# Kernel optimization log

Hardware: AMD Instinct MI355X
Metric: run time of the kernel (lower is better)

## Reference

```python
import jax, jax.numpy as jnp
import numpy as np

N = 50000      # nodes
E = 600000     # edges (avg degree 12)
D = 128        # in_dim == hidden_dim
C = 47         # n_classes
L = 3          # n_layers


def setup_inputs() -> dict:
    key = jax.random.key(0)
    ks = jax.random.split(key, 8)
    s = 1.0 / np.sqrt(D)
    return {
        "features": jax.random.normal(ks[0], (N, D), jnp.float32),
        "src": jax.random.randint(ks[1], (E,), 0, N, jnp.int32),
        "dst": jax.random.randint(ks[2], (E,), 0, N, jnp.int32),
        "w_self": jax.random.normal(ks[3], (L, D, D), jnp.float32) * s,
        "w_neigh": jax.random.normal(ks[4], (L, D, D), jnp.float32) * s,
        "b": jax.random.normal(ks[5], (L, D), jnp.float32) * s,
        "wc": jax.random.normal(ks[6], (D, C), jnp.float32) * s,
        "bc": jax.random.normal(ks[7], (C,), jnp.float32) * s,
    }


def reference(features, src, dst, w_self, w_neigh, b, wc, bc):
    # in-degree for mean aggregation (clamped to avoid div-by-zero)
    deg = jax.ops.segment_sum(jnp.ones((E,), features.dtype), dst, num_segments=N)
    inv_deg = 1.0 / jnp.maximum(deg, 1.0)  # [N]
    h = features
    for l in range(L):
        # SAGEConv (mean aggregator): gather src feats, mean-reduce onto dst
        msgs = jnp.take(h, src, axis=0)                       # [E, D]
        h_neigh = jax.ops.segment_sum(msgs, dst, num_segments=N) * inv_deg[:, None]  # [N, D]
        h = jax.nn.relu(h @ w_self[l] + h_neigh @ w_neigh[l] + b[l])
    logits = h @ wc + bc                                      # [N, C]
    return jax.nn.softmax(logits, axis=-1)
```

## Files before the change

### kernel.cpp

```cpp
#include <hip/hip_runtime.h>
#include <hip/hip_bf16.h>
#include <float.h>

#define DIM  128
#define NCLS 47
#define MAXD 64

typedef __attribute__((ext_vector_type(8))) short bf16x8;
typedef __attribute__((ext_vector_type(4))) float f32x4;

__device__ inline unsigned short bf16_rne(float v) {
  unsigned u = __float_as_uint(v);
  return (unsigned short)((u + 0x7FFFu + ((u >> 16) & 1u)) >> 16);
}

__device__ inline void split_bf16(float v, unsigned short& hi, unsigned short& lo) {
  unsigned int u = __float_as_uint(v);
  unsigned int r = (u + 0x7FFFu + ((u >> 16) & 1u)) >> 16;
  hi = (unsigned short)r;
  float hf = __uint_as_float(r << 16);
  float l = v - hf;
  unsigned int ul = __float_as_uint(l);
  unsigned int rl = (ul + 0x7FFFu + ((ul >> 16) & 1u)) >> 16;
  lo = (unsigned short)rl;
}

__device__ inline uint4 pack8(const unsigned short* h) {
  uint4 u;
  u.x = (unsigned)h[0] | ((unsigned)h[1] << 16);
  u.y = (unsigned)h[2] | ((unsigned)h[3] << 16);
  u.z = (unsigned)h[4] | ((unsigned)h[5] << 16);
  u.w = (unsigned)h[6] | ((unsigned)h[7] << 16);
  return u;
}

__global__ __launch_bounds__(256) void k_prep(const float* __restrict__ w_self,
                                              const float* __restrict__ w_neigh,
                                              const float* __restrict__ wc,
                                              const float* __restrict__ feat,
                                              uint4* __restrict__ Bhi,
                                              uint4* __restrict__ Blo,
                                              uint4* __restrict__ Chi,
                                              uint4* __restrict__ Clo,
                                              unsigned short* __restrict__ P0,
                                              unsigned short* __restrict__ P1,
                                              unsigned short* __restrict__ P2,
                                              int* __restrict__ cnt,
                                              int* __restrict__ eidx,
                                              int n, long total8) {
  int bid = blockIdx.x, tid = threadIdx.x;
  if (bid < 48) {
    int unit = bid * 4 + (tid >> 6);
    int lane = tid & 63;
    int lt = unit >> 6, rem = unit & 63, kt = rem >> 3, ct = rem & 7;
    int col = ct * 16 + (lane & 15);
    unsigned short h[8], lw[8];
#pragma unroll
    for (int j = 0; j < 8; ++j) {
      int kg = kt * 32 + (lane >> 4) * 8 + j;
      float v = (kg < 128) ? w_self[(size_t)lt * DIM * DIM + (size_t)kg * DIM + col]
                           : w_neigh[(size_t)lt * DIM * DIM + (size_t)(kg - 128) * DIM + col];
      split_bf16(v, h[j], lw[j]);
    }
    size_t idx = (((size_t)lt * 64 + kt * 8 + ct) * 64 + lane);
    Bhi[idx] = pack8(h);
    Blo[idx] = pack8(lw);
  } else if (bid < 51) {
    int unit = (bid - 48) * 4 + (tid >> 6);
    if (unit < 12) {
      int lane = tid & 63;
      int kt = unit / 3, ct = unit % 3;
      int col = ct * 16 + (lane & 15);
      unsigned short h[8], lw[8];
#pragma unroll
      for (int j = 0; j < 8; ++j) {
        int k = kt * 32 + (lane >> 4) * 8 + j;
        float v = (col < NCLS) ? wc[(size_t)k * NCLS + col] : 0.f;
        split_bf16(v, h[j], lw[j]);
      }
      size_t idx = (size_t)(kt * 3 + ct) * 64 + lane;
      Chi[idx] = pack8(h);
      Clo[idx] = pack8(lw);
    }
  } else {
    long i = (long)(bid - 51) * 256 + tid;
    if (i < n) cnt[i] = 0;
    if (i < total8) {
      const float* s = feat + i * 8;
      unsigned short h[8];
#pragma unroll
      for (int j = 0; j < 8; ++j) h[j] = bf16_rne(s[j]);
      *(uint4*)&P0[i * 8] = pack8(h);
      int4 sv = {n, n, n, n};
      ((int4*)eidx)[i] = sv;
    }
    if (bid == 51 && tid < 16) {
      uint4 z = {0u, 0u, 0u, 0u};
      ((uint4*)(P0 + (size_t)n * DIM))[tid] = z;
      ((uint4*)(P1 + (size_t)n * DIM))[tid] = z;
      ((uint4*)(P2 + (size_t)n * DIM))[tid] = z;
    }
  }
}

__global__ __launch_bounds__(256) void k_scatter4(const int* __restrict__ src,
                                                  const int* __restrict__ dst,
                                                  int* __restrict__ cnt,
                                                  int* __restrict__ eidx, int E) {
  int t = blockIdx.x * blockDim.x + threadIdx.x;
  int e0 = t * 4;
  if (e0 + 3 < E) {
    int4 d4 = *(const int4*)(dst + e0);
    int4 s4 = *(const int4*)(src + e0);
    int p0 = atomicAdd(&cnt[d4.x], 1);
    int p1 = atomicAdd(&cnt[d4.y], 1);
    int p2 = atomicAdd(&cnt[d4.z], 1);
    int p3 = atomicAdd(&cnt[d4.w], 1);
    if (p0 < MAXD) eidx[(size_t)d4.x * MAXD + p0] = s4.x;
    if (p1 < MAXD) eidx[(size_t)d4.y * MAXD + p1] = s4.y;
    if (p2 < MAXD) eidx[(size_t)d4.z * MAXD + p2] = s4.z;
    if (p3 < MAXD) eidx[(size_t)d4.w * MAXD + p3] = s4.w;
  } else {
    for (int e = e0; e < E; ++e) {
      int d = dst[e];
      int pos = atomicAdd(&cnt[d], 1);
      if (pos < MAXD) eidx[(size_t)d * MAXD + pos] = src[e];
    }
  }
}

__global__ __launch_bounds__(256) void k_agg9(const unsigned short* __restrict__ plane,
                                              unsigned short* __restrict__ hn,
                                              const int* __restrict__ cnt,
                                              const int* __restrict__ eidx, int n) {
  int node = blockIdx.x * 4 + (threadIdx.x >> 6);
  if (node >= n) return;
  int lane = threadIdx.x & 63;
  int g = lane >> 4, li = lane & 15;
  int d = cnt[node];
  int dcl = d < MAXD ? d : MAXD;
  int s = node * MAXD;
  int nch = (dcl + 15) >> 4;
  float acc[8];
#pragma unroll
  for (int k = 0; k < 8; ++k) acc[k] = 0.f;

  for (int c = 0; c < nch; ++c) {
    int base = s + c * 16 + g;
    int u0 = eidx[base];
    int u1 = eidx[base + 4];
    int u2 = eidx[base + 8];
    int u3 = eidx[base + 12];
    uint4 v0 = *(const uint4*)(plane + (size_t)u0 * DIM + li * 8);
    uint4 v1 = *(const uint4*)(plane + (size_t)u1 * DIM + li * 8);
    uint4 v2 = *(const uint4*)(plane + (size_t)u2 * DIM + li * 8);
    uint4 v3 = *(const uint4*)(plane + (size_t)u3 * DIM + li * 8);
    acc[0] += __uint_as_float(v0.x << 16); acc[1] += __uint_as_float(v0.x & 0xffff0000u);
    acc[2] += __uint_as_float(v0.y << 16); acc[3] += __uint_as_float(v0.y & 0xffff0000u);
    acc[4] += __uint_as_float(v0.z << 16); acc[5] += __uint_as_float(v0.z & 0xffff0000u);
    acc[6] += __uint_as_float(v0.w << 16); acc[7] += __uint_as_float(v0.w & 0xffff0000u);
    acc[0] += __uint_as_float(v1.x << 16); acc[1] += __uint_as_float(v1.x & 0xffff0000u);
    acc[2] += __uint_as_float(v1.y << 16); acc[3] += __uint_as_float(v1.y & 0xffff0000u);
    acc[4] += __uint_as_float(v1.z << 16); acc[5] += __uint_as_float(v1.z & 0xffff0000u);
    acc[6] += __uint_as_float(v1.w << 16); acc[7] += __uint_as_float(v1.w & 0xffff0000u);
    acc[0] += __uint_as_float(v2.x << 16); acc[1] += __uint_as_float(v2.x & 0xffff0000u);
    acc[2] += __uint_as_float(v2.y << 16); acc[3] += __uint_as_float(v2.y & 0xffff0000u);
    acc[4] += __uint_as_float(v2.z << 16); acc[5] += __uint_as_float(v2.z & 0xffff0000u);
    acc[6] += __uint_as_float(v2.w << 16); acc[7] += __uint_as_float(v2.w & 0xffff0000u);
    acc[0] += __uint_as_float(v3.x << 16); acc[1] += __uint_as_float(v3.x & 0xffff0000u);
    acc[2] += __uint_as_float(v3.y << 16); acc[3] += __uint_as_float(v3.y & 0xffff0000u);
    acc[4] += __uint_as_float(v3.z << 16); acc[5] += __uint_as_float(v3.z & 0xffff0000u);
    acc[6] += __uint_as_float(v3.w << 16); acc[7] += __uint_as_float(v3.w & 0xffff0000u);
  }
#pragma unroll
  for (int k = 0; k < 8; ++k) {
    acc[k] += __shfl_xor(acc[k], 16);
    acc[k] += __shfl_xor(acc[k], 32);
  }
  if (g == 0) {
    float idg = 1.0f / (float)(d > 1 ? d : 1);
    unsigned short hb[8];
#pragma unroll
    for (int k = 0; k < 8; ++k) hb[k] = bf16_rne(acc[k] * idg);
    *(uint4*)(hn + (size_t)node * DIM + li * 8) = pack8(hb);
  }
}

template <int LAST>
__global__ __launch_bounds__(256) void k_mm2(const unsigned short* __restrict__ plane,
                                             const unsigned short* __restrict__ hn,
                                             const uint4* __restrict__ Bhi,
                                             const uint4* __restrict__ Blo,
                                             const float* __restrict__ bias,
                                             unsigned short* __restrict__ oplane,
                                             const uint4* __restrict__ Chi,
                                             const uint4* __restrict__ Clo,
                                             const float* __restrict__ bc,
                                             float* __restrict__ out,
                                             int n) {
  __shared__ char U[34816];
  uint4* Bs = (uint4*)U;
  int tid = threadIdx.x, lane = tid & 63, w = tid >> 6;
  int rb = blockIdx.x * 128 + w * 32;

  f32x4 acc[2][8];
#pragma unroll
  for (int rf = 0; rf < 2; ++rf)
#pragma unroll
    for (int ct = 0; ct < 8; ++ct) acc[rf][ct] = (f32x4){0.f, 0.f, 0.f, 0.f};

  int r0 = rb + (lane & 15);      if (r0 > n - 1) r0 = n - 1;
  int r1 = rb + 16 + (lane & 15); if (r1 > n - 1) r1 = n - 1;
  int koff = (lane >> 4) * 8;
  const unsigned short* a0s = plane + (size_t)r0 * DIM + koff;
  const unsigned short* a1s = plane + (size_t)r1 * DIM + koff;
  const unsigned short* a0n = hn + (size_t)r0 * DIM + koff;
  const unsigned short* a1n = hn + (size_t)r1 * DIM + koff;

#define STAGE_B(kt_, buf_)                                                    \
  {                                                                           \
    const uint4* hsrc = Bhi + (size_t)(kt_) * 512;                            \
    const uint4* lsrc = Blo + (size_t)(kt_) * 512;                            \
    uint4* dstb = Bs + (size_t)(buf_) * 1024;                                 \
    dstb[tid]        = hsrc[tid];                                             \
    dstb[tid + 256]  = hsrc[tid + 256];                                       \
    dstb[tid + 512]  = lsrc[tid];                                             \
    dstb[tid + 768]  = lsrc[tid + 256];                                       \
  }

  STAGE_B(0, 0);
  __syncthreads();

#pragma unroll
  for (int kt = 0; kt < 8; ++kt) {
    if (kt < 7) STAGE_B(kt + 1, (kt + 1) & 1);
    int buf = kt & 1;
    bf16x8 a0 = (kt < 4) ? *(const bf16x8*)(a0s + kt * 32)
                         : *(const bf16x8*)(a0n + (kt - 4) * 32);
    bf16x8 a1 = (kt < 4) ? *(const bf16x8*)(a1s + kt * 32)
                         : *(const bf16x8*)(a1n + (kt - 4) * 32);
    const uint4* bb = Bs + (size_t)buf * 1024;
#pragma unroll
    for (int ct = 0; ct < 8; ++ct) {
      bf16x8 bh = *(const bf16x8*)&bb[ct * 64 + lane];
      bf16x8 bl = *(const bf16x8*)&bb[512 + ct * 64 + lane];
      acc[0][ct] = __builtin_amdgcn_mfma_f32_16x16x32_bf16(a0, bh, acc[0][ct], 0, 0, 0);
      acc[0][ct] = __builtin_amdgcn_mfma_f32_16x16x32_bf16(a0, bl, acc[0][ct], 0, 0, 0);
      acc[1][ct] = __builtin_amdgcn_mfma_f32_16x16x32_bf16(a1, bh, acc[1][ct], 0, 0, 0);
      acc[1][ct] = __builtin_amdgcn_mfma_f32_16x16x32_bf16(a1, bl, acc[1][ct], 0, 0, 0);
    }
    __syncthreads();
  }
#undef STAGE_B

  char* tw = U + (size_t)w * 32 * 272;
#pragma unroll
  for (int rf = 0; rf < 2; ++rf)
#pragma unroll
    for (int ct = 0; ct < 8; ++ct) {
      float bv = bias[ct * 16 + (lane & 15)];
#pragma unroll
      for (int q = 0; q < 4; ++q) {
        float val = fmaxf(acc[rf][ct][q] + bv, 0.f);
        int row = rf * 16 + (lane >> 4) * 4 + q;
        int key = ((row >> 2) & 3) << 5;
        int cb = (ct * 32 + (lane & 15) * 2) ^ key;
        *(unsigned short*)(tw + row * 272 + cb) = bf16_rne(val);
      }
    }

  if (!LAST) {
#pragma unroll
    for (int rr = 0; rr < 2; ++rr) {
      int r = rr * 16 + (lane >> 2);
      int grow = rb + r;
      if (grow < n) {
        int key = ((r >> 2) & 3) << 5;
        int cb0 = (lane & 3) * 64;
#pragma unroll
        for (int j = 0; j < 4; ++j) {
          uint4 v = *(const uint4*)(tw + r * 272 + ((cb0 + j * 16) ^ key));
          *(uint4*)(oplane + (size_t)grow * DIM + (cb0 + j * 16) / 2) = v;
        }
      }
    }
  } else {
#pragma unroll
    for (int rf = 0; rf < 2; ++rf) {
      f32x4 cacc[3];
#pragma unroll
      for (int ct = 0; ct < 3; ++ct) cacc[ct] = (f32x4){0.f, 0.f, 0.f, 0.f};
      int row = rf * 16 + (lane & 15);
      int key = ((row >> 2) & 3) << 5;
#pragma unroll
      for (int kt = 0; kt < 4; ++kt) {
        int bo = (kt * 64 + (lane >> 4) * 16) ^ key;
        bf16x8 a = *(const bf16x8*)(tw + row * 272 + bo);
#pragma unroll
        for (int ct = 0; ct < 3; ++ct) {
          bf16x8 bh = *(const bf16x8*)&Chi[(size_t)(kt * 3 + ct) * 64 + lane];
          bf16x8 bl = *(const bf16x8*)&Clo[(size_t)(kt * 3 + ct) * 64 + lane];
          cacc[ct] = __builtin_amdgcn_mfma_f32_16x16x32_bf16(a, bh, cacc[ct], 0, 0, 0);
          cacc[ct] = __builtin_amdgcn_mfma_f32_16x16x32_bf16(a, bl, cacc[ct], 0, 0, 0);
        }
      }
      int c0 = (lane & 15);
      int c1 = 16 + (lane & 15);
      int c2 = 32 + (lane & 15);
      bool v2 = c2 < NCLS;
      float b0 = bc[c0], b1 = bc[c1], b2 = v2 ? bc[c2] : 0.f;
#pragma unroll
      for (int q = 0; q < 4; ++q) {
        int grow = rb + rf * 16 + (lane >> 4) * 4 + q;
        float l0 = cacc[0][q] + b0;
        float l1 = cacc[1][q] + b1;
        float l2 = v2 ? cacc[2][q] + b2 : -FLT_MAX;
        float m = fmaxf(l0, fmaxf(l1, l2));
#pragma unroll
        for (int off = 8; off >= 1; off >>= 1) m = fmaxf(m, __shfl_xor(m, off));
        float e0 = __expf(l0 - m);
        float e1 = __expf(l1 - m);
        float e2 = v2 ? __expf(l2 - m) : 0.f;
        float sden = e0 + e1 + e2;
#pragma unroll
        for (int off = 8; off >= 1; off >>= 1) sden += __shfl_xor(sden, off);
        float inv = 1.0f / sden;
        if (grow < n) {
          out[(size_t)grow * NCLS + c0] = e0 * inv;
          out[(size_t)grow * NCLS + c1] = e1 * inv;
          if (v2) out[(size_t)grow * NCLS + c2] = e2 * inv;
        }
      }
    }
  }
}

extern "C" void kernel_launch(void* const* d_in, const int* in_sizes, int n_in,
                              void* d_out, int out_size, void* d_ws, size_t ws_size,
                              hipStream_t stream) {
  const float* feat   = (const float*)d_in[0];
  const int*   src    = (const int*)d_in[1];
  const int*   dst    = (const int*)d_in[2];
  const float* w_self = (const float*)d_in[3];
  const float* w_neigh= (const float*)d_in[4];
  const float* b      = (const float*)d_in[5];
  const float* wc     = (const float*)d_in[6];
  const float* bc     = (const float*)d_in[7];
  float* out = (float*)d_out;

  const int N = in_sizes[0] / DIM;
  const int E = in_sizes[1];
  const size_t PS  = (size_t)N * DIM;
  const size_t PSP = (size_t)(N + 1) * DIM;

  unsigned short* P0 = (unsigned short*)d_ws;
  unsigned short* P1 = P0 + PSP;
  unsigned short* P2 = P1 + PSP;
  unsigned short* HN = P2 + PSP;
  int*   cnt  = (int*)(HN + PS);
  int*   eidx = cnt + N;
  uintptr_t aln = ((uintptr_t)(eidx + (size_t)N * MAXD) + 255) & ~(uintptr_t)255;
  uint4* Bhi = (uint4*)aln;
  uint4* Blo = Bhi + 3 * 4096;
  uint4* Chi = Blo + 3 * 4096;
  uint4* Clo = Chi + 12 * 64;

  long total8 = (long)(PS / 8);
  int nCvt = (int)((total8 + 255) / 256);
  k_prep<<<51 + nCvt, 256, 0, stream>>>(w_self, w_neigh, wc, feat,
                                        Bhi, Blo, Chi, Clo, P0, P1, P2,
                                        cnt, eidx, N, total8);

  int nE4 = (E + 3) / 4;
  k_scatter4<<<(nE4 + 255) / 256, 256, 0, stream>>>(src, dst, cnt, eidx, E);

  const unsigned short* hin = P0;
  unsigned short* houts[2] = {P1, P2};
  for (int l = 0; l < 3; ++l) {
    k_agg9<<<(N + 3) / 4, 256, 0, stream>>>(hin, HN, cnt, eidx, N);
    if (l < 2) {
      k_mm2<0><<<(N + 127) / 128, 256, 0, stream>>>(hin, HN,
          Bhi + (size_t)l * 4096, Blo + (size_t)l * 4096,
          b + (size_t)l * DIM, houts[l], Chi, Clo, bc, out, N);
      hin = houts[l];
    } else {
      k_mm2<1><<<(N + 127) / 128, 256, 0, stream>>>(hin, HN,
          Bhi + (size_t)l * 4096, Blo + (size_t)l * 4096,
          b + (size_t)l * DIM, (unsigned short*)nullptr, Chi, Clo, bc, out, N);
    }
  }
}
```

Baseline: 177.5 us.

## Store edge indices as 16-bit and fuse edge scatter into prep kernel

Narrows the per-node neighbor index table from 32-bit to 16-bit entries, halving the table's traffic for init, scatter and all three aggregation passes. Initialization moves into a new small kernel, and the edge scatter is folded into the weight and feature conversion kernel so the two run concurrently as one launch. Node ids up to 50000 fit in 16 bits, with sentinel n=50000 also fitting. Graphs with more than 65535 nodes would silently break.

```diff
diff --git a/kernel.cpp b/kernel.cpp
--- a/kernel.cpp
+++ b/kernel.cpp
@@ -8,6 +8,7 @@
 
 typedef __attribute__((ext_vector_type(8))) short bf16x8;
 typedef __attribute__((ext_vector_type(4))) float f32x4;
+typedef unsigned short u16;
 
 __device__ inline unsigned short bf16_rne(float v) {
   unsigned u = __float_as_uint(v);
@@ -34,21 +35,66 @@
   return u;
 }
 
+__global__ __launch_bounds__(256) void k_init(u16* __restrict__ eidx,
+                                              int* __restrict__ cnt,
+                                              u16* __restrict__ P0,
+                                              u16* __restrict__ P1,
+                                              u16* __restrict__ P2,
+                                              int n, long t8) {
+  long i = (long)blockIdx.x * 256 + threadIdx.x;
+  if (i < t8) {
+    unsigned s2 = (unsigned)n | ((unsigned)n << 16);
+    uint4 v = {s2, s2, s2, s2};
+    ((uint4*)eidx)[i] = v;
+  }
+  if (i < n) cnt[i] = 0;
+  if (i < 16) {
+    uint4 z = {0u, 0u, 0u, 0u};
+    ((uint4*)(P0 + (size_t)n * DIM))[i] = z;
+    ((uint4*)(P1 + (size_t)n * DIM))[i] = z;
+    ((uint4*)(P2 + (size_t)n * DIM))[i] = z;
+  }
+}
+
 __global__ __launch_bounds__(256) void k_prep(const float* __restrict__ w_self,
                                               const float* __restrict__ w_neigh,
                                               const float* __restrict__ wc,
                                               const float* __restrict__ feat,
+                                              const int* __restrict__ src,
+                                              const int* __restrict__ dst,
                                               uint4* __restrict__ Bhi,
                                               uint4* __restrict__ Blo,
                                               uint4* __restrict__ Chi,
                                               uint4* __restrict__ Clo,
                                               unsigned short* __restrict__ P0,
-                                              unsigned short* __restrict__ P1,
-                                              unsigned short* __restrict__ P2,
                                               int* __restrict__ cnt,
-                                              int* __restrict__ eidx,
-                                              int n, long total8) {
+                                              u16* __restrict__ eidx,
+                                              int n, long total8, int E, int nS) {
   int bid = blockIdx.x, tid = threadIdx.x;
+  if (bid < nS) {
+    int t = bid * 256 + tid;
+    int e0 = t * 4;
+    if (e0 + 3 < E) {
+      int4 d4 = *(const int4*)(dst + e0);
+      int4 s4 = *(const int4*)(src + e0);
+      int p0 = atomicAdd(&cnt[d4.x], 1);
+      int p1 = atomicAdd(&cnt[d4.y], 1);
+      int p2 = atomicAdd(&cnt[d4.z], 1);
+      int p3 = atomicAdd(&cnt[d4.w], 1);
+      if (p0 < MAXD) eidx[(size_t)d4.x * MAXD + p0] = (u16)s4.x;
+      if (p1 < MAXD) eidx[(size_t)d4.y * MAXD + p1] = (u16)s4.y;
+      if (p2 < MAXD) eidx[(size_t)d4.z * MAXD + p2] = (u16)s4.z;
+      if (p3 < MAXD) eidx[(size_t)d4.w * MAXD + p3] = (u16)s4.w;
+    } else {
+      for (int e = e0; e < E; ++e) {
+        int d = dst[e];
+        int pos = atomicAdd(&cnt[d], 1);
+        if (pos < MAXD) eidx[(size_t)d * MAXD + pos] = (u16)src[e];
+      }
+    }
+    return;
+  }
+  bid -= nS;
   if (bid < 48) {
     int unit = bid * 4 + (tid >> 6);
     int lane = tid & 63;
@@ -84,47 +130,12 @@
     }
   } else {
     long i = (long)(bid - 51) * 256 + tid;
-    if (i < n) cnt[i] = 0;
     if (i < total8) {
       const float* s = feat + i * 8;
       unsigned short h[8];
 #pragma unroll
       for (int j = 0; j < 8; ++j) h[j] = bf16_rne(s[j]);
       *(uint4*)&P0[i * 8] = pack8(h);
-      int4 sv = {n, n, n, n};
-      ((int4*)eidx)[i] = sv;
-    }
-    if (bid == 51 && tid < 16) {
-      uint4 z = {0u, 0u, 0u, 0u};
-      ((uint4*)(P0 + (size_t)n * DIM))[tid] = z;
-      ((uint4*)(P1 + (size_t)n * DIM))[tid] = z;
-      ((uint4*)(P2 + (size_t)n * DIM))[tid] = z;
-    }
-  }
-}
-
-__global__ __launch_bounds__(256) void k_scatter4(const int* __restrict__ src,
-                                                  const int* __restrict__ dst,
-                                                  int* __restrict__ cnt,
-                                                  int* __restrict__ eidx, int E) {
-  int t = blockIdx.x * blockDim.x + threadIdx.x;
-  int e0 = t * 4;
-  if (e0 + 3 < E) {
-    int4 d4 = *(const int4*)(dst + e0);
-    int4 s4 = *(const int4*)(src + e0);
-    int p0 = atomicAdd(&cnt[d4.x], 1);
-    int p1 = atomicAdd(&cnt[d4.y], 1);
-    int p2 = atomicAdd(&cnt[d4.z], 1);
-    int p3 = atomicAdd(&cnt[d4.w], 1);
-    if (p0 < MAXD) eidx[(size_t)d4.x * MAXD + p0] = s4.x;
-    if (p1 < MAXD) eidx[(size_t)d4.y * MAXD + p1] = s4.y;
-    if (p2 < MAXD) eidx[(size_t)d4.z * MAXD + p2] = s4.z;
-    if (p3 < MAXD) eidx[(size_t)d4.w * MAXD + p3] = s4.w;
-  } else {
-    for (int e = e0; e < E; ++e) {
-      int d = dst[e];
-      int pos = atomicAdd(&cnt[d], 1);
-      if (pos < MAXD) eidx[(size_t)d * MAXD + pos] = src[e];
     }
   }
 }
@@ -132,7 +143,7 @@
 __global__ __launch_bounds__(256) void k_agg9(const unsigned short* __restrict__ plane,
                                               unsigned short* __restrict__ hn,
                                               const int* __restrict__ cnt,
-                                              const int* __restrict__ eidx, int n) {
+                                              const u16* __restrict__ eidx, int n) {
   int node = blockIdx.x * 4 + (threadIdx.x >> 6);
   if (node >= n) return;
   int lane = threadIdx.x & 63;
@@ -358,21 +369,24 @@
   unsigned short* P2 = P1 + PSP;
   unsigned short* HN = P2 + PSP;
   int*   cnt  = (int*)(HN + PS);
-  int*   eidx = cnt + N;
+  u16*   eidx = (u16*)(cnt + N);
   uintptr_t aln = ((uintptr_t)(eidx + (size_t)N * MAXD) + 255) & ~(uintptr_t)255;
   uint4* Bhi = (uint4*)aln;
   uint4* Blo = Bhi + 3 * 4096;
   uint4* Chi = Blo + 3 * 4096;
   uint4* Clo = Chi + 12 * 64;
 
+  long t8 = (long)N * MAXD / 8;
+  int nInit = (int)((t8 + 255) / 256);
+  k_init<<<nInit, 256, 0, stream>>>(eidx, cnt, P0, P1, P2, N, t8);
+
   long total8 = (long)(PS / 8);
   int nCvt = (int)((total8 + 255) / 256);
-  k_prep<<<51 + nCvt, 256, 0, stream>>>(w_self, w_neigh, wc, feat,
-                                        Bhi, Blo, Chi, Clo, P0, P1, P2,
-                                        cnt, eidx, N, total8);
-
   int nE4 = (E + 3) / 4;
-  k_scatter4<<<(nE4 + 255) / 256, 256, 0, stream>>>(src, dst, cnt, eidx, E);
+  int nS = (nE4 + 255) / 256;
+  k_prep<<<nS + 51 + nCvt, 256, 0, stream>>>(w_self, w_neigh, wc, feat, src, dst,
+                                             Bhi, Blo, Chi, Clo, P0,
+                                             cnt, eidx, N, total8, E, nS);
 
   const unsigned short* hin = P0;
   unsigned short* houts[2] = {P1, P2};
```

Result: no change. 177.2 us (-0.2%).
